# Optimization experiments

Measured on AMD Instinct MI355X. Metric: run time of the kernel, lower is better.

Reference implementation:

```python
import jax, jax.numpy as jnp
import numpy as np

NPOINT = 8192
NSAMPLE = 16
SUPPORT_TH = 100.0  # 10 ** 2


def sqdist(a, b):
    # a:[B,N,3], b:[B,M,3] -> squared pairwise distances [B,N,M]
    return (jnp.sum(a * a, -1)[:, :, None] + jnp.sum(b * b, -1)[:, None, :]
            - 2.0 * jnp.einsum('bnc,bmc->bnm', a, b))


def fps_single(xyz, npoint):
    # farthest point sampling; xyz:[N,3] -> [npoint] int32 indices (start at 0)
    N = xyz.shape[0]

    def body(carry, _):
        dist, far = carry
        d = jnp.sum((xyz - xyz[far]) ** 2, -1)
        dist = jnp.minimum(dist, d)
        return (dist, jnp.argmax(dist).astype(jnp.int32)), far

    init = (jnp.full((N,), 1e10, xyz.dtype), jnp.int32(0))
    _, idx = jax.lax.scan(body, init, None, length=npoint)
    return idx


def gather(p, idx):
    # p:[B,N,C], idx:[B,...] -> [B,...,C]
    return jax.vmap(lambda pp, ii: pp[ii])(p, idx)


def instance_norm(x, g, b):
    # InstanceNorm2d(affine=True): normalize over spatial dims (S,K) per (B,C)
    mu = jnp.mean(x, axis=(1, 2), keepdims=True)
    var = jnp.var(x, axis=(1, 2), keepdims=True)
    return (x - mu) / jnp.sqrt(var + 1e-5) * g + b


def set_abstraction(xyz, points, npoint, ws, gs, bs):
    # PointNetSetAbstraction, radius=None -> knn grouping. xyz:[B,3,N], points:[B,C,N]
    xt = xyz.transpose(0, 2, 1)    # [B,N,3]
    pt = points.transpose(0, 2, 1)  # [B,N,C]
    fps_idx = jax.vmap(fps_single, (0, None))(jax.lax.stop_gradient(xt), npoint)  # [B,S]
    new_xyz = gather(xt, fps_idx)                               # [B,S,3]
    d = sqdist(new_xyz, xt)                                     # [B,S,N]
    _, knn_idx = jax.lax.top_k(-d, NSAMPLE)                     # [B,S,K]
    g_xyz = gather(xt, knn_idx) - new_xyz[:, :, None, :]        # [B,S,K,3]
    g_pts = gather(pt, knn_idx)                                 # [B,S,K,C]
    x = jnp.concatenate([g_xyz, g_pts], -1)                     # [B,S,K,3+C]
    for w, g, b in zip(ws, gs, bs):                             # 1x1 conv -> IN -> relu
        x = jax.nn.relu(instance_norm(jnp.einsum('bskc,cd->bskd', x, w), g, b))
    feats = jnp.max(x, axis=2)                                  # max over nsample -> [B,S,D]
    return new_xyz.transpose(0, 2, 1), feats.transpose(0, 2, 1)


def feature_prop(xyz1, xyz2, points2):
    # PointNetFeaturePropogation with mlp=[]: 3-NN inverse-distance interpolation
    # xyz1:[B,3,N], xyz2:[B,3,S], points2:[B,C,S] -> [B,C,N]
    x1 = xyz1.transpose(0, 2, 1)
    x2 = xyz2.transpose(0, 2, 1)
    p2 = points2.transpose(0, 2, 1)
    d = sqdist(x1, x2)                       # [B,N,S]
    neg, idx = jax.lax.top_k(-d, 3)          # 3 smallest distances
    w = 1.0 / (-neg + 1e-8)
    w = w / jnp.sum(w, -1, keepdims=True)    # [B,N,3]
    nb = gather(p2, idx)                     # [B,N,3,C]
    return jnp.sum(nb * w[..., None], axis=2).transpose(0, 2, 1)


def setup_inputs() -> dict:
    key = jax.random.key(0)
    ks = jax.random.split(key, 16)
    B, N0, N1, N2, N3, CF = 8, 8192, 1024, 512, 256, 256

    def w(k, ci, co):
        return (jax.random.normal(k, (ci, co), jnp.float32) / np.sqrt(ci)).astype(jnp.float32)

    inp = {
        'pc1_l0': jax.random.normal(ks[0], (B, 3, N0), jnp.float32),
        'pc1_l1': jax.random.normal(ks[1], (B, 3, N1), jnp.float32),
        'pc1_l2': jax.random.normal(ks[2], (B, 3, N2), jnp.float32),
        'pc1_l3': jax.random.normal(ks[3], (B, 3, N3), jnp.float32),
        'pc2_l3': jax.random.normal(ks[4], (B, 3, N3), jnp.float32),
        'feats1': jax.random.normal(ks[5], (B, CF, N3), jnp.float32),
        'feats2': jax.random.normal(ks[6], (B, CF, N3), jnp.float32),
        'epsilon': jnp.zeros((1,), jnp.float32),
        'sa1_w0': w(ks[7], 6, 32), 'sa1_w1': w(ks[8], 32, 32), 'sa1_w2': w(ks[9], 32, 64),
        'sa1_g0': jnp.ones((32,), jnp.float32), 'sa1_b0': jnp.zeros((32,), jnp.float32),
        'sa1_g1': jnp.ones((32,), jnp.float32), 'sa1_b1': jnp.zeros((32,), jnp.float32),
        'sa1_g2': jnp.ones((64,), jnp.float32), 'sa1_b2': jnp.zeros((64,), jnp.float32),
        'sa2_w0': w(ks[10], 67, 64), 'sa2_w1': w(ks[11], 64, 64), 'sa2_w2': w(ks[12], 64, 128),
        'sa2_g0': jnp.ones((64,), jnp.float32), 'sa2_b0': jnp.zeros((64,), jnp.float32),
        'sa2_g1': jnp.ones((64,), jnp.float32), 'sa2_b1': jnp.zeros((64,), jnp.float32),
        'sa2_g2': jnp.ones((128,), jnp.float32), 'sa2_b2': jnp.zeros((128,), jnp.float32),
    }
    return inp


def reference(pc1_l0, pc1_l1, pc1_l2, pc1_l3, pc2_l3, feats1, feats2, epsilon,
              sa1_w0, sa1_w1, sa1_w2, sa1_g0, sa1_b0, sa1_g1, sa1_b1, sa1_g2, sa1_b2,
              sa2_w0, sa2_w1, sa2_w2, sa2_g0, sa2_b0, sa2_g1, sa2_b1, sa2_g2, sa2_b2):
    eps = jnp.exp(epsilon) + 0.03
    p1 = pc1_l3.transpose(0, 2, 1)   # [B,N3,3]
    p2 = pc2_l3.transpose(0, 2, 1)
    f1 = feats1.transpose(0, 2, 1)   # [B,N3,C]
    f2 = feats2.transpose(0, 2, 1)
    dmat = sqdist(p1, p2)
    support = (dmat < SUPPORT_TH).astype(p1.dtype)
    f1 = f1 / jnp.sqrt(jnp.sum(f1 * f1, -1, keepdims=True) + 1e-8)
    f2 = f2 / jnp.sqrt(jnp.sum(f2 * f2, -1, keepdims=True) + 1e-8)
    C = 1.0 - jnp.einsum('bnc,bmc->bnm', f1, f2)
    corr = jnp.exp(-C / eps) * support
    row = jnp.sum(corr, -1, keepdims=True)
    flow0 = jnp.einsum('bnm,bmc->bnc', corr, p2) / (row + 1e-8) - p1   # [B,N3,3]
    flow0_us = feature_prop(pc1_l2, pc1_l3, flow0.transpose(0, 2, 1))  # [B,3,N2]
    _, cf2 = set_abstraction(pc1_l2, flow0_us, NPOINT // 16,
                             (sa1_w0, sa1_w1, sa1_w2), (sa1_g0, sa1_g1, sa1_g2),
                             (sa1_b0, sa1_b1, sa1_b2))
    cf1 = feature_prop(pc1_l1, pc1_l2, cf2)
    _, cf1 = set_abstraction(pc1_l1, cf1, NPOINT // 8,
                             (sa2_w0, sa2_w1, sa2_w2), (sa2_g0, sa2_g1, sa2_g2),
                             (sa2_b0, sa2_b1, sa2_b2))
    return feature_prop(pc1_l0, pc1_l1, cf1)   # [B,128,N0]
```

## Files before the change

kernel.cpp:

```cpp
#include <hip/hip_runtime.h>
#include <math.h>

#define NB 8
#define N0 8192
#define N1 1024
#define N2 512
#define N3C 256
#define CFEAT 256
#define KNN 16
#define PSTRIDE 256

typedef float v2f __attribute__((ext_vector_type(2)));

static __device__ __forceinline__ v2f pk_add(v2f a, v2f b) {
  v2f r; asm("v_pk_add_f32 %0, %1, %2" : "=v"(r) : "v"(a), "v"(b)); return r;
}
static __device__ __forceinline__ v2f pk_mul(v2f a, v2f b) {
  v2f r; asm("v_pk_mul_f32 %0, %1, %2" : "=v"(r) : "v"(a), "v"(b)); return r;
}

template <int CTRL, int RM>
static __device__ __forceinline__ double dpp_fmax64(double m) {
  int mh = __double2hiint(m), ml = __double2loint(m);
  int ch = __builtin_amdgcn_update_dpp(mh, mh, CTRL, RM, 0xF, false);
  int cl = __builtin_amdgcn_update_dpp(ml, ml, CTRL, RM, 0xF, false);
  return fmax(m, __hiloint2double(ch, cl));
}
static __device__ __forceinline__ double wave_fmax64(double m) {
  m = dpp_fmax64<0x111, 0xF>(m);
  m = dpp_fmax64<0x112, 0xF>(m);
  m = dpp_fmax64<0x114, 0xF>(m);
  m = dpp_fmax64<0x118, 0xF>(m);
  m = dpp_fmax64<0x142, 0xA>(m);
  m = dpp_fmax64<0x143, 0xC>(m);
  return m;
}

template <int CTRL, int RM>
static __device__ __forceinline__ void dpp_minstep(uint32_t& hi, uint32_t& lo) {
  uint32_t chi = (uint32_t)__builtin_amdgcn_update_dpp((int)hi, (int)hi, CTRL, RM, 0xF, false);
  uint32_t clo = (uint32_t)__builtin_amdgcn_update_dpp((int)lo, (int)lo, CTRL, RM, 0xF, false);
  unsigned long long cand = ((unsigned long long)chi << 32) | clo;
  unsigned long long cur  = ((unsigned long long)hi  << 32) | lo;
  if (cand < cur) { hi = chi; lo = clo; }
}
static __device__ __forceinline__ void wave_min_pair(uint32_t& hi, uint32_t& lo) {
  dpp_minstep<0x111, 0xF>(hi, lo);
  dpp_minstep<0x112, 0xF>(hi, lo);
  dpp_minstep<0x114, 0xF>(hi, lo);
  dpp_minstep<0x118, 0xF>(hi, lo);
  dpp_minstep<0x142, 0xA>(hi, lo);
  dpp_minstep<0x143, 0xC>(hi, lo);
}

template <int CTRL, int RM>
static __device__ __forceinline__ float dpp_addstep(float x) {
  int xi = __float_as_int(x);
  int sv = __builtin_amdgcn_update_dpp(xi, xi, CTRL, RM, 0xF, true);
  return x + __int_as_float(sv);
}
static __device__ __forceinline__ float wave_sum63(float x) {
  x = dpp_addstep<0x111, 0xF>(x);
  x = dpp_addstep<0x112, 0xF>(x);
  x = dpp_addstep<0x114, 0xF>(x);
  x = dpp_addstep<0x118, 0xF>(x);
  x = dpp_addstep<0x142, 0xA>(x);
  x = dpp_addstep<0x143, 0xC>(x);
  return x;
}

template <int N>
static __device__ void fps_scan4(const float4* sm, double* kb, int* idx_out) {
  constexpr int PPW = N / 256;
  int tid = threadIdx.x;
  int lane = tid & 63;
  int w = tid >> 6;
  int base = w * (N / 4) + lane * PPW;
  v2f px[PPW / 2], py[PPW / 2], pz[PPW / 2];
  float dist[PPW];
  int nlo[PPW];
#pragma unroll
  for (int k = 0; k < PPW / 2; k++) {
    float4 a = sm[base + 2 * k];
    float4 c = sm[base + 2 * k + 1];
    px[k] = v2f{a.x, c.x}; py[k] = v2f{a.y, c.y}; pz[k] = v2f{a.z, c.z};
    dist[2 * k] = 1e10f; dist[2 * k + 1] = 1e10f;
    nlo[2 * k] = ~(base + 2 * k); nlo[2 * k + 1] = ~(base + 2 * k + 1);
  }
  int far = 0;
  float4 f = sm[0];
  for (int t = 0; t < N; t++) {
    if (tid == 0) idx_out[t] = far;
    v2f vfx = v2f{-f.x, -f.x}, vfy = v2f{-f.y, -f.y}, vfz = v2f{-f.z, -f.z};
#pragma unroll
    for (int k = 0; k < PPW / 2; k++) {
      v2f dx = pk_add(px[k], vfx);
      v2f dy = pk_add(py[k], vfy);
      v2f dz = pk_add(pz[k], vfz);
      v2f dd = pk_add(pk_add(pk_mul(dx, dx), pk_mul(dy, dy)), pk_mul(dz, dz));
      dist[2 * k]     = fminf(dist[2 * k],     dd.x);
      dist[2 * k + 1] = fminf(dist[2 * k + 1], dd.y);
    }
    double tv[PPW / 2];
#pragma unroll
    for (int i = 0; i < PPW / 2; i++)
      tv[i] = fmax(__hiloint2double(__float_as_int(dist[2 * i]),     nlo[2 * i]),
                   __hiloint2double(__float_as_int(dist[2 * i + 1]), nlo[2 * i + 1]));
#pragma unroll
    for (int s = PPW / 4; s >= 1; s >>= 1)
#pragma unroll
      for (int i = 0; i < s; i++) tv[i] = fmax(tv[i], tv[i + s]);
    double m = wave_fmax64(tv[0]);
    if (lane == 63) kb[(t & 1) * 4 + w] = m;
    __syncthreads();
    const double* kq = kb + (t & 1) * 4;
    double M = fmax(fmax(kq[0], kq[1]), fmax(kq[2], kq[3]));
    far = ~__double2loint(M);
    f = sm[far];
  }
}

static __device__ void corr_unit(int u, const float* __restrict__ f1, const float* __restrict__ f2,
                                 const float* __restrict__ p1, const float* __restrict__ p2,
                                 const float* __restrict__ eps_in, float* __restrict__ flow0,
                                 char* smem) {
  float* f1c = (float*)smem;
  float* red = f1c + 256;
  float* p1s = red + 16;
  int b = u / N3C, n = u % N3C;
  int m = threadIdx.x;
  f1c[m] = f1[((size_t)b * CFEAT + m) * N3C + n];
  if (m < 3) p1s[m] = p1[((size_t)b * 3 + m) * N3C + n];
  __syncthreads();
  float eps = expf(eps_in[0]) + 0.03f;
  const float* f2b = f2 + (size_t)b * CFEAT * N3C;
  float dot = 0.f, s1 = 0.f, s2 = 0.f;
  for (int c = 0; c < CFEAT; c++) {
    float a = f1c[c];
    float v = f2b[(size_t)c * N3C + m];
    dot += a * v; s1 += a * a; s2 += v * v;
  }
  float rn1 = 1.0f / sqrtf(s1 + 1e-8f);
  float rn2 = 1.0f / sqrtf(s2 + 1e-8f);
  float Cv = 1.0f - dot * rn1 * rn2;
  float p2x = p2[((size_t)b * 3 + 0) * N3C + m];
  float p2y = p2[((size_t)b * 3 + 1) * N3C + m];
  float p2z = p2[((size_t)b * 3 + 2) * N3C + m];
  float n1v = p1s[0] * p1s[0] + p1s[1] * p1s[1] + p1s[2] * p1s[2];
  float n2v = p2x * p2x + p2y * p2y + p2z * p2z;
  float dd = n1v + n2v - 2.0f * (p1s[0] * p2x + p1s[1] * p2y + p1s[2] * p2z);
  float corr = (dd < 100.0f) ? expf(-Cv / eps) : 0.0f;
  float s0 = corr, t1 = corr * p2x, t2 = corr * p2y, t3 = corr * p2z;
  for (int off = 32; off; off >>= 1) {
    s0 += __shfl_xor(s0, off, 64); t1 += __shfl_xor(t1, off, 64);
    t2 += __shfl_xor(t2, off, 64); t3 += __shfl_xor(t3, off, 64);
  }
  int wid = threadIdx.x >> 6;
  if ((threadIdx.x & 63) == 0) { red[wid] = s0; red[4 + wid] = t1; red[8 + wid] = t2; red[12 + wid] = t3; }
  __syncthreads();
  if (threadIdx.x == 0) {
    float r0 = red[0] + red[1] + red[2] + red[3];
    float r1 = red[4] + red[5] + red[6] + red[7];
    float r2 = red[8] + red[9] + red[10] + red[11];
    float r3 = red[12] + red[13] + red[14] + red[15];
    float inv = 1.0f / (r0 + 1e-8f);
    float* fo = flow0 + ((size_t)b * N3C + n) * 3;
    fo[0] = r1 * inv - p1s[0];
    fo[1] = r2 * inv - p1s[1];
    fo[2] = r3 * inv - p1s[2];
  }
  __syncthreads();
}

__global__ void fps_corr_kernel(const float* __restrict__ xyz_l2, const float* __restrict__ xyz_l1,
                                int* __restrict__ fps1, int* __restrict__ fps2,
                                const float* __restrict__ f1, const float* __restrict__ f2,
                                const float* __restrict__ p1, const float* __restrict__ p2,
                                const float* __restrict__ eps_in, float* __restrict__ flow0) {
  __shared__ __align__(16) char smem[16448];
  int blk = blockIdx.x, tid = threadIdx.x;
  if (blk < 2 * NB) {
    float4* sm = (float4*)smem;
    double* kb = (double*)(smem + 16384);
    if (blk < NB) {
      const float* xb = xyz_l2 + (size_t)blk * 3 * N2;
      for (int i = tid; i < N2; i += 256) {
        float4 v; v.x = xb[i]; v.y = xb[N2 + i]; v.z = xb[2 * N2 + i]; v.w = 0.f;
        sm[i] = v;
      }
      __syncthreads();
      fps_scan4<N2>(sm, kb, fps1 + (size_t)blk * N2);
    } else {
      int b = blk - NB;
      const float* xb = xyz_l1 + (size_t)b * 3 * N1;
      for (int i = tid; i < N1; i += 256) {
        float4 v; v.x = xb[i]; v.y = xb[N1 + i]; v.z = xb[2 * N1 + i]; v.w = 0.f;
        sm[i] = v;
      }
      __syncthreads();
      fps_scan4<N1>(sm, kb, fps2 + (size_t)b * N1);
    }
  } else {
    for (int u = blk - 2 * NB; u < NB * N3C; u += (int)gridDim.x - 2 * NB)
      corr_unit(u, f1, f2, p1, p2, eps_in, flow0, smem);
  }
}

template <int S, int PPL>
static __device__ void knn_impl(const float* __restrict__ xyz, const int* __restrict__ fps_idx,
                                int* __restrict__ knn_out, int gw) {
  int lane = threadIdx.x & 63;
  int b = gw / S, s = gw % S;
  int center = fps_idx[(size_t)b * S + s];
  const float* xb = xyz + (size_t)b * 3 * S;
  float cx = xb[center], cy = xb[S + center], cz = xb[2 * S + center];
  float cn = cx * cx + cy * cy + cz * cz;
  uint32_t kb[PPL];
#pragma unroll
  for (int j = 0; j < PPL; j++) {
    int g = lane * PPL + j;
    float x = xb[g], y = xb[S + g], z = xb[2 * S + g];
    float pn = x * x + y * y + z * z;
    float d = cn + pn - 2.0f * (cx * x + cy * y + cz * z);
    uint32_t bts = __float_as_uint(d);
    kb[j] = bts ^ ((uint32_t)((int)bts >> 31) | 0x80000000u);
  }
  int* ob = knn_out + ((size_t)b * S + s) * KNN;
  for (int r = 0; r < KNN; r++) {
    uint32_t bh = 0xFFFFFFFFu, bl = 0xFFFFFFFFu;
#pragma unroll
    for (int j = 0; j < PPL; j++) {
      unsigned long long cand = ((unsigned long long)kb[j] << 32) | (uint32_t)(lane * PPL + j);
      unsigned long long cur  = ((unsigned long long)bh << 32) | bl;
      if (cand < cur) { bh = kb[j]; bl = (uint32_t)(lane * PPL + j); }
    }
    wave_min_pair(bh, bl);
    uint32_t widx = (uint32_t)__builtin_amdgcn_readlane((int)bl, 63);
    if (lane == 0) ob[r] = (int)widx;
#pragma unroll
    for (int j = 0; j < PPL; j++)
      if ((uint32_t)(lane * PPL + j) == widx) kb[j] = 0xFFFFFFFFu;
  }
}

template <int C, bool TOUT, int S>
static __device__ void fprop_unit(int u, int Npts, const float* __restrict__ xyz1,
                                  const float* __restrict__ xyz2, const float* __restrict__ featT,
                                  float* __restrict__ out, float* smem) {
  float* x2s = smem;
  float* n2s = x2s + 3 * S;
  int tilesPerB = Npts / 256;
  int b = u / tilesPerB;
  int n = (u % tilesPerB) * 256 + threadIdx.x;
  for (int i = threadIdx.x; i < S; i += 256) {
    float xx = xyz2[((size_t)b * 3 + 0) * S + i];
    float yy = xyz2[((size_t)b * 3 + 1) * S + i];
    float zz = xyz2[((size_t)b * 3 + 2) * S + i];
    x2s[i] = xx; x2s[S + i] = yy; x2s[2 * S + i] = zz;
    n2s[i] = xx * xx + yy * yy + zz * zz;
  }
  __syncthreads();
  float X = xyz1[((size_t)b * 3 + 0) * Npts + n];
  float Y = xyz1[((size_t)b * 3 + 1) * Npts + n];
  float Z = xyz1[((size_t)b * 3 + 2) * Npts + n];
  float n1v = X * X + Y * Y + Z * Z;
  float d0 = 1e30f, d1 = 1e30f, d2 = 1e30f;
  int i0 = 0, i1 = 0, i2 = 0;
  for (int s = 0; s < S; s++) {
    float d = n1v + n2s[s] - 2.0f * (X * x2s[s] + Y * x2s[S + s] + Z * x2s[2 * S + s]);
    if (d < d0)      { d2 = d1; i2 = i1; d1 = d0; i1 = i0; d0 = d; i0 = s; }
    else if (d < d1) { d2 = d1; i2 = i1; d1 = d; i1 = s; }
    else if (d < d2) { d2 = d; i2 = s; }
  }
  float w0 = 1.0f / (d0 + 1e-8f), w1 = 1.0f / (d1 + 1e-8f), w2 = 1.0f / (d2 + 1e-8f);
  float wsum = w0 + w1 + w2;
  w0 /= wsum; w1 /= wsum; w2 /= wsum;
  const float* g0 = featT + ((size_t)b * S + i0) * C;
  const float* g1 = featT + ((size_t)b * S + i1) * C;
  const float* g2 = featT + ((size_t)b * S + i2) * C;
  if constexpr (C % 4 == 0) {
    const float4* v0 = (const float4*)g0;
    const float4* v1 = (const float4*)g1;
    const float4* v2 = (const float4*)g2;
#pragma unroll 4
    for (int c4 = 0; c4 < C / 4; c4++) {
      float4 a = v0[c4], bb = v1[c4], cc = v2[c4];
      float4 r;
      r.x = w0 * a.x + w1 * bb.x + w2 * cc.x;
      r.y = w0 * a.y + w1 * bb.y + w2 * cc.y;
      r.z = w0 * a.z + w1 * bb.z + w2 * cc.z;
      r.w = w0 * a.w + w1 * bb.w + w2 * cc.w;
      if constexpr (TOUT) {
        ((float4*)(out + ((size_t)b * Npts + n) * C))[c4] = r;
      } else {
        out[((size_t)b * C + 4 * c4 + 0) * Npts + n] = r.x;
        out[((size_t)b * C + 4 * c4 + 1) * Npts + n] = r.y;
        out[((size_t)b * C + 4 * c4 + 2) * Npts + n] = r.z;
        out[((size_t)b * C + 4 * c4 + 3) * Npts + n] = r.w;
      }
    }
  } else {
#pragma unroll
    for (int c = 0; c < C; c++) {
      float val = w0 * g0[c] + w1 * g1[c] + w2 * g2[c];
      if constexpr (TOUT) out[((size_t)b * Npts + n) * C + c] = val;
      else                out[((size_t)b * C + c) * Npts + n] = val;
    }
  }
}

__global__ void knn_fprop_kernel(const float* __restrict__ xyz_l2, const int* __restrict__ fps1,
                                 int* __restrict__ knn1,
                                 const float* __restrict__ xyz_l1, const int* __restrict__ fps2,
                                 int* __restrict__ knn2,
                                 const float* __restrict__ xyz_l3, const float* __restrict__ flow0,
                                 float* __restrict__ flow0_us) {
  __shared__ float sm[4 * N3C];
  const int KB = (NB * N2 + NB * N1) / 4;
  int blk = blockIdx.x;
  if (blk < KB) {
    int gw = blk * 4 + (threadIdx.x >> 6);
    if (gw < NB * N2) knn_impl<N2, 8>(xyz_l2, fps1, knn1, gw);
    else              knn_impl<N1, 16>(xyz_l1, fps2, knn2, gw - NB * N2);
  } else {
    fprop_unit<3, true, N3C>(blk - KB, N2, xyz_l2, xyz_l3, flow0, flow0_us, sm);
  }
}

template <int C, bool TOUT, int S>
__global__ void fprop_kernel(const float* __restrict__ xyz1, const float* __restrict__ xyz2,
                             const float* __restrict__ featT, float* __restrict__ out, int N) {
  __shared__ float sm[4 * S];
  fprop_unit<C, TOUT, S>(blockIdx.x, N, xyz1, xyz2, featT, out, sm);
}

template <int D, int DTOT, int DOFF>
static __device__ __forceinline__ void write_partials(const float* acc, int b, int bpb,
                                                      float* __restrict__ ps, float* __restrict__ pq) {
  int lane = threadIdx.x & 63;
  int slot = (blockIdx.x - b * bpb) * 4 + (threadIdx.x >> 6);
#pragma unroll
  for (int i = 0; i < D; i++) {
    float s = wave_sum63(acc[i]);
    float q = wave_sum63(acc[i] * acc[i]);
    if (lane == 63) {
      size_t row = (size_t)(b * DTOT + DOFF + i) * PSTRIDE + slot;
      ps[row] = s; pq[row] = q;
    }
  }
}

template <int CF, int D>
__global__ void mm0p_kernel(const float* __restrict__ xyz, const float* __restrict__ featsT,
                            const int* __restrict__ fps_idx, const int* __restrict__ knn,
                            const float* __restrict__ w, float* __restrict__ y,
                            float* __restrict__ ps, float* __restrict__ pq, int S) {
  const int SK = S * KNN;
  int t = blockIdx.x * 256 + threadIdx.x;
  int b = t / SK, sk = t % SK, s = sk / KNN;
  int nb = knn[(size_t)b * SK + sk];
  int ctr = fps_idx[(size_t)b * S + s];
  const float* xb = xyz + (size_t)b * 3 * S;
  float r0 = xb[nb] - xb[ctr];
  float r1 = xb[S + nb] - xb[S + ctr];
  float r2 = xb[2 * S + nb] - xb[2 * S + ctr];
  float acc[D];
#pragma unroll
  for (int i = 0; i < D; i++)
    acc[i] = fmaf(r0, w[i], fmaf(r1, w[D + i], r2 * w[2 * D + i]));
  const float* pb = featsT + ((size_t)b * S + nb) * CF;
  if constexpr (CF % 4 == 0) {
    const float4* pv = (const float4*)pb;
    for (int c4 = 0; c4 < CF / 4; c4++) {
      float4 v = pv[c4];
      const float* wr = w + (size_t)(3 + 4 * c4) * D;
#pragma unroll
      for (int i = 0; i < D; i++)
        acc[i] = fmaf(v.x, wr[i],
                 fmaf(v.y, wr[D + i],
                 fmaf(v.z, wr[2 * D + i],
                 fmaf(v.w, wr[3 * D + i], acc[i]))));
    }
  } else {
#pragma unroll
    for (int c = 0; c < CF; c++) {
      float xv = pb[c];
      const float* wr = w + (size_t)(3 + c) * D;
#pragma unroll
      for (int i = 0; i < D; i++) acc[i] = fmaf(xv, wr[i], acc[i]);
    }
  }
  float* yb = y + (size_t)b * D * SK + sk;
#pragma unroll
  for (int i = 0; i < D; i++) yb[(size_t)i * SK] = acc[i];
  write_partials<D, D, 0>(acc, b, SK / 256, ps, pq);
}

template <int Cin, int D, int DTOT, int DOFF>
__global__ void mmnorms_kernel(const float* __restrict__ x, const float* __restrict__ w,
                               const float* __restrict__ ps_in, const float* __restrict__ pq_in,
                               const float* __restrict__ g, const float* __restrict__ beta,
                               float* __restrict__ y, float* __restrict__ ps_out,
                               float* __restrict__ pq_out, int SK) {
  __shared__ float smean[Cin], srstd[Cin];
  const int NS = SK / 64;
  int b = (int)(((size_t)blockIdx.x * 256) / SK);
  {
    const int TPC = 256 / Cin;
    int c = threadIdx.x / TPC, r = threadIdx.x % TPC;
    const float* p1 = ps_in + (size_t)(b * Cin + c) * PSTRIDE;
    const float* p2 = pq_in + (size_t)(b * Cin + c) * PSTRIDE;
    float s = 0.f, q = 0.f;
    for (int j = r; j < NS; j += TPC) { s += p1[j]; q += p2[j]; }
    for (int off = TPC / 2; off; off >>= 1) {
      s += __shfl_down(s, off, 64);
      q += __shfl_down(q, off, 64);
    }
    if (r == 0) {
      float mu = s / (float)SK;
      float var = q / (float)SK - mu * mu;
      smean[c] = mu;
      srstd[c] = 1.0f / sqrtf(var + 1e-5f);
    }
  }
  __syncthreads();
  int t = blockIdx.x * 256 + threadIdx.x;
  int sk = t % SK;
  const float* xb = x + (size_t)b * Cin * SK + sk;
  float* yb = y + (size_t)b * DTOT * SK + sk;
  float acc[D];
#pragma unroll
  for (int i = 0; i < D; i++) acc[i] = 0.f;
  for (int c = 0; c < Cin; c++) {
    float sc = srstd[c] * g[c];
    float sh = fmaf(-smean[c], sc, beta[c]);
    float xv = fmaxf(fmaf(xb[(size_t)c * SK], sc, sh), 0.f);
    const float* wr = w + (size_t)c * DTOT + DOFF;
#pragma unroll
    for (int i = 0; i < D; i++) acc[i] = fmaf(xv, wr[i], acc[i]);
  }
#pragma unroll
  for (int i = 0; i < D; i++) yb[(size_t)(DOFF + i) * SK] = acc[i];
  write_partials<D, DTOT, DOFF>(acc, b, SK / 256, ps_out, pq_out);
}

template <int D>
__global__ void maxpool_norms_kernel(const float* __restrict__ y, const float* __restrict__ ps,
                                     const float* __restrict__ pq, const float* __restrict__ g,
                                     const float* __restrict__ beta, float* __restrict__ outT,
                                     int S) {
  __shared__ float sred[8];
  const int SK = S * KNN;
  const int NS = SK / 64;
  int t = blockIdx.x * 256 + threadIdx.x;
  int s = t % S;
  int bd = t / S;
  int d = bd % D, b = bd / D;
  float ssum = 0.f, qsum = 0.f;
  {
    const float* p1 = ps + (size_t)bd * PSTRIDE;
    const float* p2 = pq + (size_t)bd * PSTRIDE;
    for (int j = threadIdx.x; j < NS; j += 256) { ssum += p1[j]; qsum += p2[j]; }
    for (int off = 32; off; off >>= 1) { ssum += __shfl_xor(ssum, off, 64); qsum += __shfl_xor(qsum, off, 64); }
    int wid = threadIdx.x >> 6;
    if ((threadIdx.x & 63) == 0) { sred[wid] = ssum; sred[4 + wid] = qsum; }
    __syncthreads();
    ssum = sred[0] + sred[1] + sred[2] + sred[3];
    qsum = sred[4] + sred[5] + sred[6] + sred[7];
  }
  float mu = ssum / (float)SK;
  float var = qsum / (float)SK - mu * mu;
  float rstd = 1.0f / sqrtf(var + 1e-5f);
  float sc = rstd * g[d];
  float sh = fmaf(-mu, sc, beta[d]);
  const float4* p = (const float4*)(y + (size_t)t * KNN);
  float m = -1e30f;
#pragma unroll
  for (int q = 0; q < 4; q++) {
    float4 v = p[q];
    m = fmaxf(m, fmaf(v.x, sc, sh)); m = fmaxf(m, fmaf(v.y, sc, sh));
    m = fmaxf(m, fmaf(v.z, sc, sh)); m = fmaxf(m, fmaf(v.w, sc, sh));
  }
  outT[((size_t)b * S + s) * D + d] = fmaxf(m, 0.f);
}

extern "C" void kernel_launch(void* const* d_in, const int* in_sizes, int n_in,
                              void* d_out, int out_size, void* d_ws, size_t ws_size,
                              hipStream_t stream) {
  const float* pc1_l0 = (const float*)d_in[0];
  const float* pc1_l1 = (const float*)d_in[1];
  const float* pc1_l2 = (const float*)d_in[2];
  const float* pc1_l3 = (const float*)d_in[3];
  const float* pc2_l3 = (const float*)d_in[4];
  const float* feats1 = (const float*)d_in[5];
  const float* feats2 = (const float*)d_in[6];
  const float* epsilon = (const float*)d_in[7];
  const float* sa1_w[3] = {(const float*)d_in[8], (const float*)d_in[9], (const float*)d_in[10]};
  const float* sa1_g[3] = {(const float*)d_in[11], (const float*)d_in[13], (const float*)d_in[15]};
  const float* sa1_b[3] = {(const float*)d_in[12], (const float*)d_in[14], (const float*)d_in[16]};
  const float* sa2_w[3] = {(const float*)d_in[17], (const float*)d_in[18], (const float*)d_in[19]};
  const float* sa2_g[3] = {(const float*)d_in[20], (const float*)d_in[22], (const float*)d_in[24]};
  const float* sa2_b[3] = {(const float*)d_in[21], (const float*)d_in[23], (const float*)d_in[25]};

  char* ws = (char*)d_ws;
  size_t off = 0;
  auto alloc = [&](size_t bytes) { char* p = ws + off; off += (bytes + 255) & ~(size_t)255; return p; };
  float* bigA     = (float*)alloc((size_t)NB * 128 * N1 * KNN * 4);
  float* bigB     = (float*)alloc((size_t)NB * 64 * N1 * KNN * 4);
  float* psA      = (float*)alloc((size_t)NB * 128 * PSTRIDE * 4);
  float* pqA      = (float*)alloc((size_t)NB * 128 * PSTRIDE * 4);
  float* psB      = (float*)alloc((size_t)NB * 128 * PSTRIDE * 4);
  float* pqB      = (float*)alloc((size_t)NB * 128 * PSTRIDE * 4);
  float* flow0    = (float*)alloc((size_t)NB * N3C * 3 * 4);
  float* flow0_us = (float*)alloc((size_t)NB * N2 * 3 * 4);
  int*   fps1     = (int*)alloc((size_t)NB * N2 * 4);
  int*   knn1     = (int*)alloc((size_t)NB * N2 * KNN * 4);
  float* cf2      = (float*)alloc((size_t)NB * N2 * 64 * 4);
  float* cf1a     = (float*)alloc((size_t)NB * N1 * 64 * 4);
  int*   fps2     = (int*)alloc((size_t)NB * N1 * 4);
  int*   knn2     = (int*)alloc((size_t)NB * N1 * KNN * 4);
  float* cf1b     = (float*)alloc((size_t)NB * N1 * 128 * 4);
  (void)ws_size; (void)in_sizes; (void)n_in; (void)out_size;

  fps_corr_kernel<<<2 * NB + 2048, 256, 0, stream>>>(pc1_l2, pc1_l1, fps1, fps2,
                                                     feats1, feats2, pc1_l3, pc2_l3,
                                                     epsilon, flow0);

  knn_fprop_kernel<<<(NB * N2 + NB * N1) / 4 + NB * (N2 / 256), 256, 0, stream>>>(
      pc1_l2, fps1, knn1, pc1_l1, fps2, knn2, pc1_l3, flow0, flow0_us);

  {
    const int S = N2, SK = S * KNN;
    const int G = NB * SK / 256;
    mm0p_kernel<3, 32><<<G, 256, 0, stream>>>(pc1_l2, flow0_us, fps1, knn1, sa1_w[0],
                                              bigA, psA, pqA, S);
    mmnorms_kernel<32, 32, 32, 0><<<G, 256, 0, stream>>>(bigA, sa1_w[1], psA, pqA,
                                                         sa1_g[0], sa1_b[0],
                                                         bigB, psB, pqB, SK);
    mmnorms_kernel<32, 64, 64, 0><<<G, 256, 0, stream>>>(bigB, sa1_w[2], psB, pqB,
                                                         sa1_g[1], sa1_b[1],
                                                         bigA, psA, pqA, SK);
    maxpool_norms_kernel<64><<<NB * 64 * S / 256, 256, 0, stream>>>(bigA, psA, pqA,
                                                                    sa1_g[2], sa1_b[2], cf2, S);
  }

  fprop_kernel<64, true, N2><<<NB * (N1 / 256), 256, 0, stream>>>(pc1_l1, pc1_l2, cf2, cf1a, N1);

  {
    const int S = N1, SK = S * KNN;
    const int G = NB * SK / 256;
    mm0p_kernel<64, 64><<<G, 256, 0, stream>>>(pc1_l1, cf1a, fps2, knn2, sa2_w[0],
                                               bigA, psA, pqA, S);
    mmnorms_kernel<64, 64, 64, 0><<<G, 256, 0, stream>>>(bigA, sa2_w[1], psA, pqA,
                                                         sa2_g[0], sa2_b[0],
                                                         bigB, psB, pqB, SK);
    mmnorms_kernel<64, 64, 128, 0><<<G, 256, 0, stream>>>(bigB, sa2_w[2], psB, pqB,
                                                          sa2_g[1], sa2_b[1],
                                                          bigA, psA, pqA, SK);
    mmnorms_kernel<64, 64, 128, 64><<<G, 256, 0, stream>>>(bigB, sa2_w[2], psB, pqB,
                                                           sa2_g[1], sa2_b[1],
                                                           bigA, psA, pqA, SK);
    maxpool_norms_kernel<128><<<NB * 128 * S / 256, 256, 0, stream>>>(bigA, psA, pqA,
                                                                      sa2_g[2], sa2_b[2], cf1b, S);
  }

  fprop_kernel<128, false, N1><<<NB * (N0 / 256), 256, 0, stream>>>(pc1_l0, pc1_l1, cf1b,
                                                                    (float*)d_out, N0);
}
```

Before: 857.4 us.

## Widen FPS blocks to 512 threads, pair corr units, merge split mmnorms launches

```diff
diff --git a/kernel.cpp b/kernel.cpp
--- a/kernel.cpp
+++ b/kernel.cpp
@@ -19,6 +19,10 @@
   v2f r; asm("v_pk_mul_f32 %0, %1, %2" : "=v"(r) : "v"(a), "v"(b)); return r;
 }
 
+static __device__ __forceinline__ float sq3(float dx, float dy, float dz) {
+  return __fadd_rn(__fadd_rn(__fmul_rn(dx, dx), __fmul_rn(dy, dy)), __fmul_rn(dz, dz));
+}
+
 template <int CTRL, int RM>
 static __device__ __forceinline__ double dpp_fmax64(double m) {
   int mh = __double2hiint(m), ml = __double2loint(m);
@@ -70,65 +74,73 @@
 }
 
 template <int N>
-static __device__ void fps_scan4(const float4* sm, double* kb, int* idx_out) {
-  constexpr int PPW = N / 256;
+static __device__ void fps_scan8(const float4* sm, double* kb, int* idx_out) {
+  constexpr int PPW = N / 512;
   int tid = threadIdx.x;
   int lane = tid & 63;
   int w = tid >> 6;
-  int base = w * (N / 4) + lane * PPW;
-  v2f px[PPW / 2], py[PPW / 2], pz[PPW / 2];
-  float dist[PPW];
-  int nlo[PPW];
-#pragma unroll
-  for (int k = 0; k < PPW / 2; k++) {
-    float4 a = sm[base + 2 * k];
-    float4 c = sm[base + 2 * k + 1];
-    px[k] = v2f{a.x, c.x}; py[k] = v2f{a.y, c.y}; pz[k] = v2f{a.z, c.z};
-    dist[2 * k] = 1e10f; dist[2 * k + 1] = 1e10f;
-    nlo[2 * k] = ~(base + 2 * k); nlo[2 * k + 1] = ~(base + 2 * k + 1);
-  }
+  int base = w * (N / 8) + lane * PPW;
   int far = 0;
   float4 f = sm[0];
-  for (int t = 0; t < N; t++) {
-    if (tid == 0) idx_out[t] = far;
-    v2f vfx = v2f{-f.x, -f.x}, vfy = v2f{-f.y, -f.y}, vfz = v2f{-f.z, -f.z};
-#pragma unroll
-    for (int k = 0; k < PPW / 2; k++) {
-      v2f dx = pk_add(px[k], vfx);
-      v2f dy = pk_add(py[k], vfy);
-      v2f dz = pk_add(pz[k], vfz);
+  if constexpr (PPW == 1) {
+    float4 a = sm[base];
+    float px = a.x, py = a.y, pz = a.z;
+    float dist = 1e10f;
+    int nlo = ~base;
+    for (int t = 0; t < N; t++) {
+      if (tid == 0) idx_out[t] = far;
+      float d = sq3(px - f.x, py - f.y, pz - f.z);
+      dist = fminf(dist, d);
+      double m = wave_fmax64(__hiloint2double(__float_as_int(dist), nlo));
+      if (lane == 63) kb[(t & 1) * 8 + w] = m;
+      __syncthreads();
+      const double* kq = kb + (t & 1) * 8;
+      double m0 = fmax(kq[0], kq[1]), m1 = fmax(kq[2], kq[3]);
+      double m2 = fmax(kq[4], kq[5]), m3 = fmax(kq[6], kq[7]);
+      double M = fmax(fmax(m0, m1), fmax(m2, m3));
+      far = ~__double2loint(M);
+      f = sm[far];
+    }
+  } else {
+    float4 a = sm[base], c = sm[base + 1];
+    v2f px = v2f{a.x, c.x}, py = v2f{a.y, c.y}, pz = v2f{a.z, c.z};
+    float d0v = 1e10f, d1v = 1e10f;
+    int n0 = ~base, n1 = ~(base + 1);
+    for (int t = 0; t < N; t++) {
+      if (tid == 0) idx_out[t] = far;
+      v2f vfx = v2f{-f.x, -f.x}, vfy = v2f{-f.y, -f.y}, vfz = v2f{-f.z, -f.z};
+      v2f dx = pk_add(px, vfx);
+      v2f dy = pk_add(py, vfy);
+      v2f dz = pk_add(pz, vfz);
       v2f dd = pk_add(pk_add(pk_mul(dx, dx), pk_mul(dy, dy)), pk_mul(dz, dz));
-      dist[2 * k]     = fminf(dist[2 * k],     dd.x);
-      dist[2 * k + 1] = fminf(dist[2 * k + 1], dd.y);
-    }
-    double tv[PPW / 2];
-#pragma unroll
-    for (int i = 0; i < PPW / 2; i++)
-      tv[i] = fmax(__hiloint2double(__float_as_int(dist[2 * i]),     nlo[2 * i]),
-                   __hiloint2double(__float_as_int(dist[2 * i + 1]), nlo[2 * i + 1]));
-#pragma unroll
-    for (int s = PPW / 4; s >= 1; s >>= 1)
-#pragma unroll
-      for (int i = 0; i < s; i++) tv[i] = fmax(tv[i], tv[i + s]);
-    double m = wave_fmax64(tv[0]);
-    if (lane == 63) kb[(t & 1) * 4 + w] = m;
-    __syncthreads();
-    const double* kq = kb + (t & 1) * 4;
-    double M = fmax(fmax(kq[0], kq[1]), fmax(kq[2], kq[3]));
-    far = ~__double2loint(M);
-    f = sm[far];
-  }
-}
-
-static __device__ void corr_unit(int u, const float* __restrict__ f1, const float* __restrict__ f2,
-                                 const float* __restrict__ p1, const float* __restrict__ p2,
-                                 const float* __restrict__ eps_in, float* __restrict__ flow0,
-                                 char* smem) {
-  float* f1c = (float*)smem;
+      d0v = fminf(d0v, dd.x);
+      d1v = fminf(d1v, dd.y);
+      double tv = fmax(__hiloint2double(__float_as_int(d0v), n0),
+                       __hiloint2double(__float_as_int(d1v), n1));
+      double m = wave_fmax64(tv);
+      if (lane == 63) kb[(t & 1) * 8 + w] = m;
+      __syncthreads();
+      const double* kq = kb + (t & 1) * 8;
+      double m0 = fmax(kq[0], kq[1]), m1 = fmax(kq[2], kq[3]);
+      double m2 = fmax(kq[4], kq[5]), m3 = fmax(kq[6], kq[7]);
+      double M = fmax(fmax(m0, m1), fmax(m2, m3));
+      far = ~__double2loint(M);
+      f = sm[far];
+    }
+  }
+}
+
+static __device__ void corr_unit2(int u0, const float* __restrict__ f1, const float* __restrict__ f2,
+                                  const float* __restrict__ p1, const float* __restrict__ p2,
+                                  const float* __restrict__ eps_in, float* __restrict__ flow0,
+                                  char* smem) {
+  int half = threadIdx.x >> 8;
+  int m = threadIdx.x & 255;
+  int u = u0 + half;
+  float* f1c = (float*)smem + half * 280;
   float* red = f1c + 256;
   float* p1s = red + 16;
   int b = u / N3C, n = u % N3C;
-  int m = threadIdx.x;
   f1c[m] = f1[((size_t)b * CFEAT + m) * N3C + n];
   if (m < 3) p1s[m] = p1[((size_t)b * 3 + m) * N3C + n];
   __syncthreads();
@@ -155,10 +167,10 @@
     s0 += __shfl_xor(s0, off, 64); t1 += __shfl_xor(t1, off, 64);
     t2 += __shfl_xor(t2, off, 64); t3 += __shfl_xor(t3, off, 64);
   }
-  int wid = threadIdx.x >> 6;
-  if ((threadIdx.x & 63) == 0) { red[wid] = s0; red[4 + wid] = t1; red[8 + wid] = t2; red[12 + wid] = t3; }
+  int wid = m >> 6;
+  if ((m & 63) == 0) { red[wid] = s0; red[4 + wid] = t1; red[8 + wid] = t2; red[12 + wid] = t3; }
   __syncthreads();
-  if (threadIdx.x == 0) {
+  if (m == 0) {
     float r0 = red[0] + red[1] + red[2] + red[3];
     float r1 = red[4] + red[5] + red[6] + red[7];
     float r2 = red[8] + red[9] + red[10] + red[11];
@@ -177,32 +189,32 @@
                                 const float* __restrict__ f1, const float* __restrict__ f2,
                                 const float* __restrict__ p1, const float* __restrict__ p2,
                                 const float* __restrict__ eps_in, float* __restrict__ flow0) {
-  __shared__ __align__(16) char smem[16448];
+  __shared__ __align__(16) char smem[16384 + 128];
   int blk = blockIdx.x, tid = threadIdx.x;
   if (blk < 2 * NB) {
     float4* sm = (float4*)smem;
     double* kb = (double*)(smem + 16384);
     if (blk < NB) {
       const float* xb = xyz_l2 + (size_t)blk * 3 * N2;
-      for (int i = tid; i < N2; i += 256) {
+      for (int i = tid; i < N2; i += 512) {
         float4 v; v.x = xb[i]; v.y = xb[N2 + i]; v.z = xb[2 * N2 + i]; v.w = 0.f;
         sm[i] = v;
       }
       __syncthreads();
-      fps_scan4<N2>(sm, kb, fps1 + (size_t)blk * N2);
+      fps_scan8<N2>(sm, kb, fps1 + (size_t)blk * N2);
     } else {
       int b = blk - NB;
       const float* xb = xyz_l1 + (size_t)b * 3 * N1;
-      for (int i = tid; i < N1; i += 256) {
+      for (int i = tid; i < N1; i += 512) {
         float4 v; v.x = xb[i]; v.y = xb[N1 + i]; v.z = xb[2 * N1 + i]; v.w = 0.f;
         sm[i] = v;
       }
       __syncthreads();
-      fps_scan4<N1>(sm, kb, fps2 + (size_t)b * N1);
+      fps_scan8<N1>(sm, kb, fps2 + (size_t)b * N1);
     }
   } else {
-    for (int u = blk - 2 * NB; u < NB * N3C; u += (int)gridDim.x - 2 * NB)
-      corr_unit(u, f1, f2, p1, p2, eps_in, flow0, smem);
+    for (int u0 = (blk - 2 * NB) * 2; u0 < NB * N3C; u0 += ((int)gridDim.x - 2 * NB) * 2)
+      corr_unit2(u0, f1, f2, p1, p2, eps_in, flow0, smem);
   }
 }
 
@@ -334,17 +346,18 @@
   fprop_unit<C, TOUT, S>(blockIdx.x, N, xyz1, xyz2, featT, out, sm);
 }
 
-template <int D, int DTOT, int DOFF>
-static __device__ __forceinline__ void write_partials(const float* acc, int b, int bpb,
+template <int D>
+static __device__ __forceinline__ void write_partials(const float* acc, int b, int bpb, int blk,
+                                                      int dtot, int doff,
                                                       float* __restrict__ ps, float* __restrict__ pq) {
   int lane = threadIdx.x & 63;
-  int slot = (blockIdx.x - b * bpb) * 4 + (threadIdx.x >> 6);
+  int slot = (blk - b * bpb) * 4 + (threadIdx.x >> 6);
 #pragma unroll
   for (int i = 0; i < D; i++) {
     float s = wave_sum63(acc[i]);
     float q = wave_sum63(acc[i] * acc[i]);
     if (lane == 63) {
-      size_t row = (size_t)(b * DTOT + DOFF + i) * PSTRIDE + slot;
+      size_t row = (size_t)(b * dtot + doff + i) * PSTRIDE + slot;
       ps[row] = s; pq[row] = q;
     }
   }
@@ -393,18 +406,21 @@
   float* yb = y + (size_t)b * D * SK + sk;
 #pragma unroll
   for (int i = 0; i < D; i++) yb[(size_t)i * SK] = acc[i];
-  write_partials<D, D, 0>(acc, b, SK / 256, ps, pq);
-}
-
-template <int Cin, int D, int DTOT, int DOFF>
+  write_partials<D>(acc, b, SK / 256, blockIdx.x, D, 0, ps, pq);
+}
+
+template <int Cin, int D, int DTOT>
 __global__ void mmnorms_kernel(const float* __restrict__ x, const float* __restrict__ w,
                                const float* __restrict__ ps_in, const float* __restrict__ pq_in,
                                const float* __restrict__ g, const float* __restrict__ beta,
                                float* __restrict__ y, float* __restrict__ ps_out,
-                               float* __restrict__ pq_out, int SK) {
+                               float* __restrict__ pq_out, int SK, int G) {
   __shared__ float smean[Cin], srstd[Cin];
   const int NS = SK / 64;
-  int b = (int)(((size_t)blockIdx.x * 256) / SK);
+  int blk = blockIdx.x;
+  int doff = 0;
+  if (blk >= G) { blk -= G; doff = D; }
+  int b = (int)(((size_t)blk * 256) / SK);
   {
     const int TPC = 256 / Cin;
     int c = threadIdx.x / TPC, r = threadIdx.x % TPC;
@@ -424,7 +440,7 @@
     }
   }
   __syncthreads();
-  int t = blockIdx.x * 256 + threadIdx.x;
+  int t = blk * 256 + threadIdx.x;
   int sk = t % SK;
   const float* xb = x + (size_t)b * Cin * SK + sk;
   float* yb = y + (size_t)b * DTOT * SK + sk;
@@ -435,13 +451,13 @@
     float sc = srstd[c] * g[c];
     float sh = fmaf(-smean[c], sc, beta[c]);
     float xv = fmaxf(fmaf(xb[(size_t)c * SK], sc, sh), 0.f);
-    const float* wr = w + (size_t)c * DTOT + DOFF;
+    const float* wr = w + (size_t)c * DTOT + doff;
 #pragma unroll
     for (int i = 0; i < D; i++) acc[i] = fmaf(xv, wr[i], acc[i]);
   }
 #pragma unroll
-  for (int i = 0; i < D; i++) yb[(size_t)(DOFF + i) * SK] = acc[i];
-  write_partials<D, DTOT, DOFF>(acc, b, SK / 256, ps_out, pq_out);
+  for (int i = 0; i < D; i++) yb[(size_t)(doff + i) * SK] = acc[i];
+  write_partials<D>(acc, b, SK / 256, blk, DTOT, doff, ps_out, pq_out);
 }
 
 template <int D>
@@ -522,7 +538,7 @@
   float* cf1b     = (float*)alloc((size_t)NB * N1 * 128 * 4);
   (void)ws_size; (void)in_sizes; (void)n_in; (void)out_size;
 
-  fps_corr_kernel<<<2 * NB + 2048, 256, 0, stream>>>(pc1_l2, pc1_l1, fps1, fps2,
+  fps_corr_kernel<<<2 * NB + 1024, 512, 0, stream>>>(pc1_l2, pc1_l1, fps1, fps2,
                                                      feats1, feats2, pc1_l3, pc2_l3,
                                                      epsilon, flow0);
 
@@ -534,12 +550,12 @@
     const int G = NB * SK / 256;
     mm0p_kernel<3, 32><<<G, 256, 0, stream>>>(pc1_l2, flow0_us, fps1, knn1, sa1_w[0],
                                               bigA, psA, pqA, S);
-    mmnorms_kernel<32, 32, 32, 0><<<G, 256, 0, stream>>>(bigA, sa1_w[1], psA, pqA,
-                                                         sa1_g[0], sa1_b[0],
-                                                         bigB, psB, pqB, SK);
-    mmnorms_kernel<32, 64, 64, 0><<<G, 256, 0, stream>>>(bigB, sa1_w[2], psB, pqB,
-                                                         sa1_g[1], sa1_b[1],
-                                                         bigA, psA, pqA, SK);
+    mmnorms_kernel<32, 32, 32><<<G, 256, 0, stream>>>(bigA, sa1_w[1], psA, pqA,
+                                                      sa1_g[0], sa1_b[0],
+                                                      bigB, psB, pqB, SK, G);
+    mmnorms_kernel<32, 64, 64><<<G, 256, 0, stream>>>(bigB, sa1_w[2], psB, pqB,
+                                                      sa1_g[1], sa1_b[1],
+                                                      bigA, psA, pqA, SK, G);
     maxpool_norms_kernel<64><<<NB * 64 * S / 256, 256, 0, stream>>>(bigA, psA, pqA,
                                                                     sa1_g[2], sa1_b[2], cf2, S);
   }
@@ -551,15 +567,12 @@
     const int G = NB * SK / 256;
     mm0p_kernel<64, 64><<<G, 256, 0, stream>>>(pc1_l1, cf1a, fps2, knn2, sa2_w[0],
                                                bigA, psA, pqA, S);
-    mmnorms_kernel<64, 64, 64, 0><<<G, 256, 0, stream>>>(bigA, sa2_w[1], psA, pqA,
-                                                         sa2_g[0], sa2_b[0],
-                                                         bigB, psB, pqB, SK);
-    mmnorms_kernel<64, 64, 128, 0><<<G, 256, 0, stream>>>(bigB, sa2_w[2], psB, pqB,
-                                                          sa2_g[1], sa2_b[1],
-                                                          bigA, psA, pqA, SK);
-    mmnorms_kernel<64, 64, 128, 64><<<G, 256, 0, stream>>>(bigB, sa2_w[2], psB, pqB,
+    mmnorms_kernel<64, 64, 64><<<G, 256, 0, stream>>>(bigA, sa2_w[1], psA, pqA,
+                                                      sa2_g[0], sa2_b[0],
+                                                      bigB, psB, pqB, SK, G);
+    mmnorms_kernel<64, 64, 128><<<2 * G, 256, 0, stream>>>(bigB, sa2_w[2], psB, pqB,
                                                            sa2_g[1], sa2_b[1],
-                                                           bigA, psA, pqA, SK);
+                                                           bigA, psA, pqA, SK, G);
     maxpool_norms_kernel<128><<<NB * 128 * S / 256, 256, 0, stream>>>(bigA, psA, pqA,
                                                                       sa2_g[2], sa2_b[2], cf1b, S);
   }
```

After: 891.0 us. 1.04x slower.
